# Optimization experiments

Measured on AMD Instinct MI355X. Metric: run time of the kernel, lower is better.

## Reference

```python
import jax, jax.numpy as jnp
import numpy as np

D = 12          # tree depth; N = 2**D - 1 = 4095 nodes per tree (heap layout)
B = 64          # batch of trees
V = 128         # VOCAB_SIZE (one-hot token width)
H = 256         # hidden_size
NUM_OPS = 20
TEMP = 3.0      # self.temperature


def setup_inputs() -> dict:
    key = jax.random.key(0)
    ks = jax.random.split(key, 9)
    s = 0.02
    return {
        "arg_hot": jax.random.uniform(ks[0], (B, 2**D - 1, V), dtype=jnp.float32),
        "Wiou": jax.random.normal(ks[1], (V, 3 * H), dtype=jnp.float32) * s,
        "biou": jnp.zeros((3 * H,), jnp.float32),
        "Uiou": jax.random.normal(ks[2], (2, H, 3 * H), dtype=jnp.float32) * s,
        "Wf": jax.random.normal(ks[3], (V, H), dtype=jnp.float32) * s,
        "bf": jnp.zeros((H,), jnp.float32),
        "Uf": jax.random.normal(ks[4], (2, 2, H, H), dtype=jnp.float32) * s,
        "actor_w": jax.random.normal(ks[5], (NUM_OPS, H), dtype=jnp.float32) * s,
        "actor_b": jnp.zeros((NUM_OPS,), jnp.float32),
        "validity_mask": jnp.ones((B, NUM_OPS), jnp.float32),
    }


def _binary_tree_lstm(arg_hot, Wiou, biou, Uiou, Wf, bf, Uf):
    """Levelized apply_binary_lstm: bottom-up N-ary (N=2) Tree-LSTM over a
    complete binary tree stored in heap order (children of node j at level l
    are positions 2j, 2j+1 of level l+1). Missing children (below leaves)
    contribute zero hidden/cell states, matching self.tz in the original."""
    Bn = arg_hot.shape[0]
    h_child = c_child = None
    h = c = None
    for l in reversed(range(D)):
        m = 2 ** l
        x = arg_hot[:, m - 1: 2 * m - 1]                    # [B, m, V]
        if h_child is None:  # leaf level: zero child states
            hk = jnp.zeros((2, Bn, m, H), arg_hot.dtype)
            ck = hk
        else:                # children 2j, 2j+1 are adjacent pairs
            hk = h_child.reshape(Bn, m, 2, H).transpose(2, 0, 1, 3)  # [2,B,m,H]
            ck = c_child.reshape(Bn, m, 2, H).transpose(2, 0, 1, 3)
        iou = (jnp.einsum('bmv,vg->bmg', x, Wiou) + biou
               + jnp.einsum('kbmh,khg->bmg', hk, Uiou))     # [B,m,3H]
        i, o, u = jnp.split(iou, 3, axis=-1)
        i, o, u = jax.nn.sigmoid(i), jax.nn.sigmoid(o), jnp.tanh(u)
        # per-child forget gates f_k = sigma(Wf x + sum_j Uf[k,j] h_j + bf)
        f = jax.nn.sigmoid(jnp.einsum('bmv,vh->bmh', x, Wf) + bf
                           + jnp.einsum('jbmh,kjhd->kbmd', hk, Uf))  # [2,B,m,H]
        c = i * u + jnp.sum(f * ck, axis=0)                 # [B,m,H]
        h = o * jnp.tanh(c)
        h_child, c_child = h, c
    return h[:, 0], c[:, 0]                                  # root states [B,H]


def reference(arg_hot, Wiou, biou, Uiou, Wf, bf, Uf, actor_w, actor_b, validity_mask):
    root_h, _ = _binary_tree_lstm(arg_hot, Wiou, biou, Uiou, Wf, bf, Uf)
    # external-actor branch of policy(): mask weights/bias, add log-mask, tempered softmax
    w = actor_w[None, :, :] * validity_mask[:, :, None]      # [B,O,H]
    b = actor_b[None, :] * validity_mask                     # [B,O]
    logits = jnp.log(validity_mask) + jnp.einsum('bh,boh->bo', root_h, w) + b
    return jax.nn.softmax(logits / TEMP, axis=-1)
```

## Files before the change

kernel.cpp:

```cpp
#include <hip/hip_runtime.h>
#include <hip/hip_bf16.h>
#include <math.h>

typedef __hip_bfloat16 bf16;
typedef float f32x4 __attribute__((ext_vector_type(4)));
typedef short bf16x8 __attribute__((ext_vector_type(8)));

#define NNODES 4095
#define BATCH 64
#define NUM_OPS 20
#define TEMP 3.0f

#define OFF_WTILE 0x000000ull
#define OFF_WTL   0x190000ull
#define OFF_BIAS  0x1C0000ull
#define OFF_HA    0x200000ull
#define OFF_CA    (OFF_HA + (64ull<<20))
#define OFF_HB    (OFF_CA + (64ull<<20))
#define OFF_CB    (OFF_HB + (32ull<<20))
#define OFF_XL    OFF_HB

__device__ __forceinline__ float sigmoid_f(float x) {
    return 1.0f / (1.0f + __expf(-x));
}
__device__ __forceinline__ float tanh_f(float x) {
    return 1.0f - 2.0f / (__expf(2.0f * x) + 1.0f);
}

__device__ __forceinline__ void async_copy16(const bf16* g, bf16* l) {
    __builtin_amdgcn_global_load_lds(
        (const __attribute__((address_space(1))) void*)g,
        (__attribute__((address_space(3))) void*)l,
        16, 0, 0);
}

__global__ void init_weights(const float* __restrict__ Wiou,
                             const float* __restrict__ biou,
                             const float* __restrict__ Uiou,
                             const float* __restrict__ Wf,
                             const float* __restrict__ bfv,
                             const float* __restrict__ Uf,
                             bf16* __restrict__ wtile,
                             bf16* __restrict__ wtL,
                             float* __restrict__ biasCat)
{
    int idx = blockIdx.x * 256 + threadIdx.x;
    if (idx < 1280 * 640) {
        int k = idx % 640;
        int n = idx / 640;
        int g = n >> 8;
        int ch = n & 255;
        float v;
        if (k < 128) {
            v = (g < 3) ? Wiou[k * 768 + n] : Wf[k * 256 + ch];
        } else {
            int par = (k < 384) ? 0 : 1;
            int hh = (k - 128) & 255;
            if (g < 3) v = Uiou[(par * 256 + hh) * 768 + n];
            else {
                int kk = g - 3;
                v = Uf[(((kk * 2 + par) * 256) + hh) * 256 + ch];
            }
        }
        bf16 bv = __float2bfloat16(v);
        int chblk = (ch >> 5);
        int cl    = ch & 31;
        int kb    = k >> 6;
        int chunk = (k & 63) >> 3;
        int e     = k & 7;
        int brow  = g * 32 + cl;
        wtile[((size_t)(chblk * 10 + kb) * 8 + chunk) * 1280 + brow * 8 + e] = bv;
        if (k < 128 && g < 3)
            wtL[((size_t)(chblk * 2 + kb) * 8 + chunk) * 768 + brow * 8 + e] = bv;
    }
    if (idx < 1280) {
        biasCat[idx] = (idx < 768) ? biou[idx] : bfv[idx & 255];
    }
}

__global__ void convert_x(const float* __restrict__ arg_hot, bf16* __restrict__ xL)
{
    int t = blockIdx.x * 256 + threadIdx.x;
    int row = t >> 4;
    int ch0 = (t & 15) * 8;
    int b = row >> 11;
    int j = row & 2047;
    const float* src = arg_hot + ((size_t)b * NNODES + 2047 + j) * 128 + ch0;
    float4 a = *(const float4*)src;
    float4 c = *(const float4*)(src + 4);
    union { bf16x8 v; __hip_bfloat162 h2[4]; } u;
    u.h2[0] = __float22bfloat162_rn(make_float2(a.x, a.y));
    u.h2[1] = __float22bfloat162_rn(make_float2(a.z, a.w));
    u.h2[2] = __float22bfloat162_rn(make_float2(c.x, c.y));
    u.h2[3] = __float22bfloat162_rn(make_float2(c.z, c.w));
    *(bf16x8*)(xL + (size_t)t * 8) = u.v;
}

template <bool LEAF>
__global__ __launch_bounds__(256, 2)
void level_kernel(const float* __restrict__ arg_hot,
                  const bf16* __restrict__ wt,
                  const float* __restrict__ biasCat,
                  const bf16* __restrict__ xL,
                  const bf16* __restrict__ h_child,
                  const bf16* __restrict__ c_child,
                  bf16* __restrict__ h_out,
                  bf16* __restrict__ c_out,
                  int m, int logm)
{
    constexpr int NG  = LEAF ? 3 : 5;
    constexpr int KI  = LEAF ? 2 : 10;
    constexpr int BR  = LEAF ? 96 : 160;
    constexpr int NBW = LEAF ? 3 : 5;

    const int M = BATCH * m;
    const int node_base = m - 1;

    __shared__ bf16 As[2][128 * 64];
    __shared__ bf16 Bs[2][8 * BR * 8];

    const int tid = threadIdx.x;

    int bid = blockIdx.x;
    int mtiles = gridDim.x >> 3;
    int mtile, chblk;
    if ((mtiles & 7) == 0) {
        int xcd = bid & 7;
        int seq = bid >> 3;
        chblk = seq & 7;
        mtile = ((seq >> 3) << 3) + xcd;
    } else {
        mtile = bid >> 3;
        chblk = bid & 7;
    }
    const int rbase  = mtile * 128;
    const int chbase = chblk * 32;

    const int lane = tid & 63;
    const int wave = tid >> 6;
    const int wr = wave & 1;
    const int wc = wave >> 1;
    const int l15 = lane & 15;
    const int lq  = lane >> 4;
    const int xr7 = l15 & 7;

    f32x4 acc[4][NG];
#pragma unroll
    for (int a = 0; a < 4; ++a)
#pragma unroll
        for (int g = 0; g < NG; ++g)
            acc[a][g] = (f32x4){0.f, 0.f, 0.f, 0.f};

    const int row_l = lane >> 3;
    const int cc_l  = lane & 7;
    const int aoffH = row_l * 512 + (cc_l ^ row_l) * 8;
    const int aoffX = row_l * 128 + (cc_l ^ row_l) * 8;

    const bf16* wbase = wt + (size_t)chblk * KI * (BR * 64);

    const int arow = tid & 127;
    const int rs = min(rbase + arow, M - 1);
    const float* xrow = LEAF ? nullptr : arg_hot +
        ((size_t)(rs >> logm) * NNODES + node_base + (rs & (m - 1))) * 128;
    const int xswz_base = arow * 64;
    const int ar7 = arow & 7;

    const bf16* xLbase = LEAF ? xL + (size_t)rbase * 128 + aoffX : nullptr;

    auto stage = [&](int kb, int buf) {
        bf16* Ab = As[buf];
        bf16* Bb = Bs[buf];
        if (LEAF) {
            const bf16* xb = xLbase + kb * 64;
#pragma unroll
            for (int i = 0; i < 4; ++i) {
                int t = wave * 4 + i;
                async_copy16(xb + t * 1024, &Ab[t * 512]);
            }
        } else if (kb < 2) {
            const float* xk = xrow + kb * 64;
#pragma unroll
            for (int j = 0; j < 4; ++j) {
                int chunk = (tid >> 7) + 2 * j;
                const float* src = xk + chunk * 8;
                float4 a = *(const float4*)src;
                float4 b = *(const float4*)(src + 4);
                union { int4 i4; __hip_bfloat162 h2[4]; } u;
                u.h2[0] = __float22bfloat162_rn(make_float2(a.x, a.y));
                u.h2[1] = __float22bfloat162_rn(make_float2(a.z, a.w));
                u.h2[2] = __float22bfloat162_rn(make_float2(b.x, b.y));
                u.h2[3] = __float22bfloat162_rn(make_float2(b.z, b.w));
                *(int4*)&Ab[xswz_base + ((chunk ^ ar7) * 8)] = u.i4;
            }
        } else {
            const bf16* hb = h_child + (size_t)rbase * 512 + (kb * 64 - 128) + aoffH;
#pragma unroll
            for (int i = 0; i < 4; ++i) {
                int t = wave * 4 + i;
                async_copy16(hb + t * 8 * 512, &Ab[t * 512]);
            }
        }
        const bf16* bsrc = wbase + (size_t)kb * (BR * 64);
#pragma unroll
        for (int i = 0; i < NBW; ++i) {
            int t = wave * NBW + i;
            async_copy16(bsrc + t * 512 + lane * 8, &Bb[t * 512]);
        }
    };

    stage(0, 0);

    for (int kb = 0; kb < KI; ++kb) {
        int buf = kb & 1;
        __syncthreads();
        if (kb + 1 < KI) stage(kb + 1, buf ^ 1);
#pragma unroll
        for (int ks = 0; ks < 2; ++ks) {
            int q = ks * 4 + lq;
            int qa = (q ^ xr7) * 8;
            bf16x8 af[4];
#pragma unroll
            for (int rt = 0; rt < 4; ++rt)
                af[rt] = *(const bf16x8*)&As[buf][(wr * 64 + rt * 16 + l15) * 64 + qa];
#pragma unroll
            for (int g = 0; g < NG; ++g) {
                bf16x8 bfr = *(const bf16x8*)&Bs[buf][q * (BR * 8) + (g * 32 + wc * 16 + l15) * 8];
#pragma unroll
                for (int rt = 0; rt < 4; ++rt)
                    acc[rt][g] = __builtin_amdgcn_mfma_f32_16x16x32_bf16(
                        af[rt], bfr, acc[rt][g], 0, 0, 0);
            }
        }
    }

    const int ch = chbase + wc * 16 + l15;
    const float b_i = biasCat[ch];
    const float b_o = biasCat[256 + ch];
    const float b_u = biasCat[512 + ch];
    const float b_f = LEAF ? 0.f : biasCat[768 + ch];

#pragma unroll
    for (int rt = 0; rt < 4; ++rt) {
#pragma unroll
        for (int ri = 0; ri < 4; ++ri) {
            int r = rbase + wr * 64 + rt * 16 + lq * 4 + ri;
            if (r < M) {
                float i = sigmoid_f(acc[rt][0][ri] + b_i);
                float o = sigmoid_f(acc[rt][1][ri] + b_o);
                float u = tanh_f(acc[rt][2][ri] + b_u);
                float cn;
                if (LEAF) {
                    cn = i * u;
                } else {
                    float f0 = sigmoid_f(acc[rt][3][ri] + b_f);
                    float f1 = sigmoid_f(acc[rt][4][ri] + b_f);
                    float c0 = __bfloat162float(c_child[(size_t)r * 512 + ch]);
                    float c1 = __bfloat162float(c_child[(size_t)r * 512 + 256 + ch]);
                    cn = i * u + f0 * c0 + f1 * c1;
                }
                float h = o * tanh_f(cn);
                h_out[(size_t)r * 256 + ch] = __float2bfloat16(h);
                c_out[(size_t)r * 256 + ch] = __float2bfloat16(cn);
            }
        }
    }
}

__global__ void head_kernel(const bf16* __restrict__ rootH,
                            const float* __restrict__ actor_w,
                            const float* __restrict__ actor_b,
                            const float* __restrict__ vmask,
                            float* __restrict__ out)
{
    int b = blockIdx.x;
    __shared__ float logits[NUM_OPS];
    int t = threadIdx.x;
    if (t < NUM_OPS) {
        const bf16* hr = rootH + b * 256;
        const float* w = actor_w + t * 256;
        float dot = 0.f;
        for (int hh = 0; hh < 256; ++hh)
            dot += __bfloat162float(hr[hh]) * w[hh];
        float mk = vmask[b * NUM_OPS + t];
        float lg = (mk > 0.f) ? (logf(mk) + (dot + actor_b[t]) * mk) : -INFINITY;
        logits[t] = lg / TEMP;
    }
    __syncthreads();
    if (t == 0) {
        float mx = -INFINITY;
        for (int o = 0; o < NUM_OPS; ++o) mx = fmaxf(mx, logits[o]);
        float s = 0.f;
        float e[NUM_OPS];
        for (int o = 0; o < NUM_OPS; ++o) { e[o] = __expf(logits[o] - mx); s += e[o]; }
        float inv = 1.f / s;
        for (int o = 0; o < NUM_OPS; ++o) out[b * NUM_OPS + o] = e[o] * inv;
    }
}

extern "C" void kernel_launch(void* const* d_in, const int* in_sizes, int n_in,
                              void* d_out, int out_size, void* d_ws, size_t ws_size,
                              hipStream_t stream)
{
    const float* arg_hot = (const float*)d_in[0];
    const float* Wiou    = (const float*)d_in[1];
    const float* biou    = (const float*)d_in[2];
    const float* Uiou    = (const float*)d_in[3];
    const float* Wf      = (const float*)d_in[4];
    const float* bfv     = (const float*)d_in[5];
    const float* Uf      = (const float*)d_in[6];
    const float* actor_w = (const float*)d_in[7];
    const float* actor_b = (const float*)d_in[8];
    const float* vmask   = (const float*)d_in[9];

    char* ws = (char*)d_ws;
    bf16*  wtile   = (bf16*)(ws + OFF_WTILE);
    bf16*  wtL     = (bf16*)(ws + OFF_WTL);
    float* biasCat = (float*)(ws + OFF_BIAS);
    bf16*  hA = (bf16*)(ws + OFF_HA);
    bf16*  cA = (bf16*)(ws + OFF_CA);
    bf16*  hB = (bf16*)(ws + OFF_HB);
    bf16*  cB = (bf16*)(ws + OFF_CB);
    bf16*  xL = (bf16*)(ws + OFF_XL);

    init_weights<<<dim3((1280 * 640 + 255) / 256), 256, 0, stream>>>(
        Wiou, biou, Uiou, Wf, bfv, Uf, wtile, wtL, biasCat);
    convert_x<<<dim3(8192), 256, 0, stream>>>(arg_hot, xL);

    {
        int m = 2048;
        int mtiles = (BATCH * m + 127) / 128;
        level_kernel<true><<<dim3(mtiles * 8), 256, 0, stream>>>(
            arg_hot, wtL, biasCat, xL, nullptr, nullptr, hA, cA, m, 11);
    }
    for (int l = 10; l >= 0; --l) {
        int m = 1 << l;
        int mtiles = (BATCH * m + 127) / 128;
        bf16 *hc, *cc, *ho, *co;
        if (l & 1) { hc = hB; cc = cB; ho = hA; co = cA; }
        else       { hc = hA; cc = cA; ho = hB; co = cB; }
        level_kernel<false><<<dim3(mtiles * 8), 256, 0, stream>>>(
            arg_hot, wtile, biasCat, nullptr, hc, cc, ho, co, m, l);
    }
    head_kernel<<<dim3(BATCH), 64, 0, stream>>>(hB, actor_w, actor_b, vmask, (float*)d_out);
}
```

Before: 835.1 us.

## Split gate groups across two wave groups in 512-thread level kernel

Doubles the level kernel block to 512 threads. One group of four waves computes the i/o/u gate GEMMs and the other computes the two forget gates (for leaves: i,u vs o). Partial results are exchanged through shared memory reused from the A tile, with an extra barrier in the epilogue. The aim is to cut the accumulator registers per wave and raise the number of resident waves for latency hiding. The cost is an uneven 3:2 split of MFMA work, an extra barrier, and shared-memory traffic in the epilogue.

```diff
diff --git a/kernel.cpp b/kernel.cpp
--- a/kernel.cpp
+++ b/kernel.cpp
@@ -97,7 +97,7 @@
 }
 
 template <bool LEAF>
-__global__ __launch_bounds__(256, 2)
+__global__ __launch_bounds__(512, 4)
 void level_kernel(const float* __restrict__ arg_hot,
                   const bf16* __restrict__ wt,
                   const float* __restrict__ biasCat,
@@ -108,10 +108,11 @@
                   bf16* __restrict__ c_out,
                   int m, int logm)
 {
-    constexpr int NG  = LEAF ? 3 : 5;
     constexpr int KI  = LEAF ? 2 : 10;
     constexpr int BR  = LEAF ? 96 : 160;
-    constexpr int NBW = LEAF ? 3 : 5;
+    constexpr int BI  = LEAF ? 12 : 20;
+    constexpr int NG0 = LEAF ? 2 : 3;
+    constexpr int NG1 = LEAF ? 1 : 2;
 
     const int M = BATCH * m;
     const int node_base = m - 1;
@@ -139,16 +140,17 @@
     const int lane = tid & 63;
     const int wave = tid >> 6;
     const int wr = wave & 1;
-    const int wc = wave >> 1;
+    const int wc = (wave >> 1) & 1;
+    const int wg = wave >> 2;
     const int l15 = lane & 15;
     const int lq  = lane >> 4;
     const int xr7 = l15 & 7;
 
-    f32x4 acc[4][NG];
+    f32x4 acc[4][3];
 #pragma unroll
     for (int a = 0; a < 4; ++a)
 #pragma unroll
-        for (int g = 0; g < NG; ++g)
+        for (int g = 0; g < 3; ++g)
             acc[a][g] = (f32x4){0.f, 0.f, 0.f, 0.f};
 
     const int row_l = lane >> 3;
@@ -173,15 +175,15 @@
         if (LEAF) {
             const bf16* xb = xLbase + kb * 64;
 #pragma unroll
-            for (int i = 0; i < 4; ++i) {
-                int t = wave * 4 + i;
+            for (int jj = 0; jj < 2; ++jj) {
+                int t = wave * 2 + jj;
                 async_copy16(xb + t * 1024, &Ab[t * 512]);
             }
         } else if (kb < 2) {
             const float* xk = xrow + kb * 64;
 #pragma unroll
-            for (int j = 0; j < 4; ++j) {
-                int chunk = (tid >> 7) + 2 * j;
+            for (int jj = 0; jj < 2; ++jj) {
+                int chunk = (tid >> 7) + 4 * jj;
                 const float* src = xk + chunk * 8;
                 float4 a = *(const float4*)src;
                 float4 b = *(const float4*)(src + 4);
@@ -195,17 +197,14 @@
         } else {
             const bf16* hb = h_child + (size_t)rbase * 512 + (kb * 64 - 128) + aoffH;
 #pragma unroll
-            for (int i = 0; i < 4; ++i) {
-                int t = wave * 4 + i;
+            for (int jj = 0; jj < 2; ++jj) {
+                int t = wave * 2 + jj;
                 async_copy16(hb + t * 8 * 512, &Ab[t * 512]);
             }
         }
         const bf16* bsrc = wbase + (size_t)kb * (BR * 64);
-#pragma unroll
-        for (int i = 0; i < NBW; ++i) {
-            int t = wave * NBW + i;
-            async_copy16(bsrc + t * 512 + lane * 8, &Bb[t * 512]);
-        }
+        for (int j = wave; j < BI; j += 8)
+            async_copy16(bsrc + j * 512 + lane * 8, &Bb[j * 512]);
     };
 
     stage(0, 0);
@@ -222,46 +221,108 @@
 #pragma unroll
             for (int rt = 0; rt < 4; ++rt)
                 af[rt] = *(const bf16x8*)&As[buf][(wr * 64 + rt * 16 + l15) * 64 + qa];
-#pragma unroll
-            for (int g = 0; g < NG; ++g) {
-                bf16x8 bfr = *(const bf16x8*)&Bs[buf][q * (BR * 8) + (g * 32 + wc * 16 + l15) * 8];
-#pragma unroll
-                for (int rt = 0; rt < 4; ++rt)
-                    acc[rt][g] = __builtin_amdgcn_mfma_f32_16x16x32_bf16(
-                        af[rt], bfr, acc[rt][g], 0, 0, 0);
+            if (wg == 0) {
+#pragma unroll
+                for (int gi = 0; gi < NG0; ++gi) {
+                    int g = LEAF ? gi * 2 : gi;
+                    bf16x8 bfr = *(const bf16x8*)&Bs[buf][q * (BR * 8) + (g * 32 + wc * 16 + l15) * 8];
+#pragma unroll
+                    for (int rt = 0; rt < 4; ++rt)
+                        acc[rt][gi] = __builtin_amdgcn_mfma_f32_16x16x32_bf16(
+                            af[rt], bfr, acc[rt][gi], 0, 0, 0);
+                }
+            } else {
+#pragma unroll
+                for (int gi = 0; gi < NG1; ++gi) {
+                    int g = LEAF ? 1 : 3 + gi;
+                    bf16x8 bfr = *(const bf16x8*)&Bs[buf][q * (BR * 8) + (g * 32 + wc * 16 + l15) * 8];
+#pragma unroll
+                    for (int rt = 0; rt < 4; ++rt)
+                        acc[rt][gi] = __builtin_amdgcn_mfma_f32_16x16x32_bf16(
+                            af[rt], bfr, acc[rt][gi], 0, 0, 0);
+                }
             }
         }
     }
 
     const int ch = chbase + wc * 16 + l15;
-    const float b_i = biasCat[ch];
-    const float b_o = biasCat[256 + ch];
-    const float b_u = biasCat[512 + ch];
-    const float b_f = LEAF ? 0.f : biasCat[768 + ch];
-
-#pragma unroll
-    for (int rt = 0; rt < 4; ++rt) {
-#pragma unroll
-        for (int ri = 0; ri < 4; ++ri) {
-            int r = rbase + wr * 64 + rt * 16 + lq * 4 + ri;
-            if (r < M) {
-                float i = sigmoid_f(acc[rt][0][ri] + b_i);
-                float o = sigmoid_f(acc[rt][1][ri] + b_o);
-                float u = tanh_f(acc[rt][2][ri] + b_u);
-                float cn;
-                if (LEAF) {
-                    cn = i * u;
-                } else {
-                    float f0 = sigmoid_f(acc[rt][3][ri] + b_f);
-                    float f1 = sigmoid_f(acc[rt][4][ri] + b_f);
-                    float c0 = __bfloat162float(c_child[(size_t)r * 512 + ch]);
-                    float c1 = __bfloat162float(c_child[(size_t)r * 512 + 256 + ch]);
-                    cn = i * u + f0 * c0 + f1 * c1;
-                }
-                float h = o * tanh_f(cn);
-                h_out[(size_t)r * 256 + ch] = __float2bfloat16(h);
-                c_out[(size_t)r * 256 + ch] = __float2bfloat16(cn);
-            }
+    float* fs = (float*)(&As[0][0]);
+    const int sbase = (wr * 2 + wc) * 64 + lane;
+
+    if (!LEAF) {
+        if (wg == 1) {
+            const float b_f = biasCat[768 + ch];
+#pragma unroll
+            for (int rt = 0; rt < 4; ++rt)
+#pragma unroll
+                for (int ri = 0; ri < 4; ++ri) {
+                    int r = rbase + wr * 64 + rt * 16 + lq * 4 + ri;
+                    float v = 0.f;
+                    if (r < M) {
+                        float f0 = sigmoid_f(acc[rt][0][ri] + b_f);
+                        float f1 = sigmoid_f(acc[rt][1][ri] + b_f);
+                        float c0 = __bfloat162float(c_child[(size_t)r * 512 + ch]);
+                        float c1 = __bfloat162float(c_child[(size_t)r * 512 + 256 + ch]);
+                        v = f0 * c0 + f1 * c1;
+                    }
+                    fs[(rt * 4 + ri) * 256 + sbase] = v;
+                }
+        }
+        __syncthreads();
+        if (wg == 0) {
+            const float b_i = biasCat[ch];
+            const float b_o = biasCat[256 + ch];
+            const float b_u = biasCat[512 + ch];
+#pragma unroll
+            for (int rt = 0; rt < 4; ++rt)
+#pragma unroll
+                for (int ri = 0; ri < 4; ++ri) {
+                    int r = rbase + wr * 64 + rt * 16 + lq * 4 + ri;
+                    if (r < M) {
+                        float i = sigmoid_f(acc[rt][0][ri] + b_i);
+                        float o = sigmoid_f(acc[rt][1][ri] + b_o);
+                        float u = tanh_f(acc[rt][2][ri] + b_u);
+                        float cn = i * u + fs[(rt * 4 + ri) * 256 + sbase];
+                        float h = o * tanh_f(cn);
+                        h_out[(size_t)r * 256 + ch] = __float2bfloat16(h);
+                        c_out[(size_t)r * 256 + ch] = __float2bfloat16(cn);
+                    }
+                }
+        }
+    } else {
+        if (wg == 0) {
+            const float b_i = biasCat[ch];
+            const float b_u = biasCat[512 + ch];
+#pragma unroll
+            for (int rt = 0; rt < 4; ++rt)
+#pragma unroll
+                for (int ri = 0; ri < 4; ++ri) {
+                    int r = rbase + wr * 64 + rt * 16 + lq * 4 + ri;
+                    float cn = 0.f;
+                    if (r < M) {
+                        float i = sigmoid_f(acc[rt][0][ri] + b_i);
+                        float u = tanh_f(acc[rt][1][ri] + b_u);
+                        cn = i * u;
+                        c_out[(size_t)r * 256 + ch] = __float2bfloat16(cn);
+                    }
+                    fs[(rt * 4 + ri) * 256 + sbase] = cn;
+                }
+        }
+        __syncthreads();
+        if (wg == 1) {
+            const float b_o = biasCat[256 + ch];
+#pragma unroll
+            for (int rt = 0; rt < 4; ++rt)
+#pragma unroll
+                for (int ri = 0; ri < 4; ++ri) {
+                    int r = rbase + wr * 64 + rt * 16 + lq * 4 + ri;
+                    if (r < M) {
+                        float o = sigmoid_f(acc[rt][0][ri] + b_o);
+                        float cn = fs[(rt * 4 + ri) * 256 + sbase];
+                        float h = o * tanh_f(cn);
+                        h_out[(size_t)r * 256 + ch] = __float2bfloat16(h);
+                    }
+                }
         }
     }
 }
@@ -329,7 +390,7 @@
     {
         int m = 2048;
         int mtiles = (BATCH * m + 127) / 128;
-        level_kernel<true><<<dim3(mtiles * 8), 256, 0, stream>>>(
+        level_kernel<true><<<dim3(mtiles * 8), 512, 0, stream>>>(
             arg_hot, wtL, biasCat, xL, nullptr, nullptr, hA, cA, m, 11);
     }
     for (int l = 10; l >= 0; --l) {
@@ -338,7 +399,7 @@
         bf16 *hc, *cc, *ho, *co;
         if (l & 1) { hc = hB; cc = cB; ho = hA; co = cA; }
         else       { hc = hA; cc = cA; ho = hB; co = cB; }
-        level_kernel<false><<<dim3(mtiles * 8), 256, 0, stream>>>(
+        level_kernel<false><<<dim3(mtiles * 8), 512, 0, stream>>>(
             arg_hot, wtile, biasCat, nullptr, hc, cc, ho, co, m, l);
     }
     head_kernel<<<dim3(BATCH), 64, 0, stream>>>(hB, actor_w, actor_b, vmask, (float*)d_out);
```

Result: slower. 984.3 us (+17.9%).

## Halve K tile to 32 and shrink LDS to allow four blocks per CU

Applied to the files above, without the earlier changes.

Halves the K-dimension tile from 64 to 32. The weight tiles are repacked into matching 32-wide chunks, the A-tile swizzle is reworked for 32-element rows, and shared-memory buffers are halved. Launch bounds are raised from 2 to 4 blocks per CU so more waves can hide memory latency. The cost is twice as many pipeline iterations and barriers per GEMM, and a tighter register budget that could cause spills given the 20-accumulator array.

```diff
diff --git a/kernel.cpp b/kernel.cpp
--- a/kernel.cpp
+++ b/kernel.cpp
@@ -65,13 +65,13 @@
         bf16 bv = __float2bfloat16(v);
         int chblk = (ch >> 5);
         int cl    = ch & 31;
-        int kb    = k >> 6;
-        int chunk = (k & 63) >> 3;
+        int kb    = k >> 5;
+        int chunk = (k & 31) >> 3;
         int e     = k & 7;
         int brow  = g * 32 + cl;
-        wtile[((size_t)(chblk * 10 + kb) * 8 + chunk) * 1280 + brow * 8 + e] = bv;
+        wtile[((size_t)(chblk * 20 + kb) * 4 + chunk) * 1280 + brow * 8 + e] = bv;
         if (k < 128 && g < 3)
-            wtL[((size_t)(chblk * 2 + kb) * 8 + chunk) * 768 + brow * 8 + e] = bv;
+            wtL[((size_t)(chblk * 4 + kb) * 4 + chunk) * 768 + brow * 8 + e] = bv;
     }
     if (idx < 1280) {
         biasCat[idx] = (idx < 768) ? biou[idx] : bfv[idx & 255];
@@ -97,7 +97,7 @@
 }
 
 template <bool LEAF>
-__global__ __launch_bounds__(256, 2)
+__global__ __launch_bounds__(256, 4)
 void level_kernel(const float* __restrict__ arg_hot,
                   const bf16* __restrict__ wt,
                   const float* __restrict__ biasCat,
@@ -109,15 +109,15 @@
                   int m, int logm)
 {
     constexpr int NG  = LEAF ? 3 : 5;
-    constexpr int KI  = LEAF ? 2 : 10;
+    constexpr int KI  = LEAF ? 4 : 20;
     constexpr int BR  = LEAF ? 96 : 160;
-    constexpr int NBW = LEAF ? 3 : 5;
+    constexpr int BI  = LEAF ? 6 : 10;
 
     const int M = BATCH * m;
     const int node_base = m - 1;
 
-    __shared__ bf16 As[2][128 * 64];
-    __shared__ bf16 Bs[2][8 * BR * 8];
+    __shared__ bf16 As[2][128 * 32];
+    __shared__ bf16 Bs[2][4 * BR * 8];
 
     const int tid = threadIdx.x;
 
@@ -142,7 +142,7 @@
     const int wc = wave >> 1;
     const int l15 = lane & 15;
     const int lq  = lane >> 4;
-    const int xr7 = l15 & 7;
+    const int xr3 = (l15 >> 1) & 3;
 
     f32x4 acc[4][NG];
 #pragma unroll
@@ -151,19 +151,19 @@
         for (int g = 0; g < NG; ++g)
             acc[a][g] = (f32x4){0.f, 0.f, 0.f, 0.f};
 
-    const int row_l = lane >> 3;
-    const int cc_l  = lane & 7;
-    const int aoffH = row_l * 512 + (cc_l ^ row_l) * 8;
-    const int aoffX = row_l * 128 + (cc_l ^ row_l) * 8;
-
-    const bf16* wbase = wt + (size_t)chblk * KI * (BR * 64);
+    const int l4 = lane >> 2;
+    const int c4 = lane & 3;
+    const int akey  = (l4 >> 1) & 3;
+    const int aoffH = l4 * 512 + (c4 ^ akey) * 8;
+    const int aoffX = l4 * 128 + (c4 ^ akey) * 8;
+
+    const bf16* wbase = wt + (size_t)chblk * KI * (BR * 32);
 
     const int arow = tid & 127;
     const int rs = min(rbase + arow, M - 1);
     const float* xrow = LEAF ? nullptr : arg_hot +
         ((size_t)(rs >> logm) * NNODES + node_base + (rs & (m - 1))) * 128;
-    const int xswz_base = arow * 64;
-    const int ar7 = arow & 7;
+    const int ar3 = (arow >> 1) & 3;
 
     const bf16* xLbase = LEAF ? xL + (size_t)rbase * 128 + aoffX : nullptr;
 
@@ -171,18 +171,18 @@
         bf16* Ab = As[buf];
         bf16* Bb = Bs[buf];
         if (LEAF) {
-            const bf16* xb = xLbase + kb * 64;
-#pragma unroll
-            for (int i = 0; i < 4; ++i) {
-                int t = wave * 4 + i;
-                async_copy16(xb + t * 1024, &Ab[t * 512]);
-            }
-        } else if (kb < 2) {
-            const float* xk = xrow + kb * 64;
-#pragma unroll
-            for (int j = 0; j < 4; ++j) {
-                int chunk = (tid >> 7) + 2 * j;
-                const float* src = xk + chunk * 8;
+            const bf16* xb = xLbase + kb * 32;
+#pragma unroll
+            for (int i = 0; i < 2; ++i) {
+                int t = wave * 2 + i;
+                async_copy16(xb + t * 2048, &Ab[t * 512]);
+            }
+        } else if (kb < 4) {
+            const float* xk = xrow + kb * 32;
+#pragma unroll
+            for (int j = 0; j < 2; ++j) {
+                int c = (tid >> 7) + 2 * j;
+                const float* src = xk + c * 8;
                 float4 a = *(const float4*)src;
                 float4 b = *(const float4*)(src + 4);
                 union { int4 i4; __hip_bfloat162 h2[4]; } u;
@@ -190,22 +190,19 @@
                 u.h2[1] = __float22bfloat162_rn(make_float2(a.z, a.w));
                 u.h2[2] = __float22bfloat162_rn(make_float2(b.x, b.y));
                 u.h2[3] = __float22bfloat162_rn(make_float2(b.z, b.w));
-                *(int4*)&Ab[xswz_base + ((chunk ^ ar7) * 8)] = u.i4;
+                *(int4*)&Ab[arow * 32 + ((c ^ ar3) * 8)] = u.i4;
             }
         } else {
-            const bf16* hb = h_child + (size_t)rbase * 512 + (kb * 64 - 128) + aoffH;
-#pragma unroll
-            for (int i = 0; i < 4; ++i) {
-                int t = wave * 4 + i;
-                async_copy16(hb + t * 8 * 512, &Ab[t * 512]);
+            const bf16* hb = h_child + (size_t)rbase * 512 + (kb * 32 - 128) + aoffH;
+#pragma unroll
+            for (int i = 0; i < 2; ++i) {
+                int t = wave * 2 + i;
+                async_copy16(hb + (size_t)t * 16 * 512, &Ab[t * 512]);
             }
         }
-        const bf16* bsrc = wbase + (size_t)kb * (BR * 64);
-#pragma unroll
-        for (int i = 0; i < NBW; ++i) {
-            int t = wave * NBW + i;
-            async_copy16(bsrc + t * 512 + lane * 8, &Bb[t * 512]);
-        }
+        const bf16* bsrc = wbase + (size_t)kb * (BR * 32);
+        for (int j = wave; j < BI; j += 4)
+            async_copy16(bsrc + j * 512 + lane * 8, &Bb[j * 512]);
     };
 
     stage(0, 0);
@@ -214,22 +211,17 @@
         int buf = kb & 1;
         __syncthreads();
         if (kb + 1 < KI) stage(kb + 1, buf ^ 1);
-#pragma unroll
-        for (int ks = 0; ks < 2; ++ks) {
-            int q = ks * 4 + lq;
-            int qa = (q ^ xr7) * 8;
-            bf16x8 af[4];
+        bf16x8 af[4];
+#pragma unroll
+        for (int rt = 0; rt < 4; ++rt)
+            af[rt] = *(const bf16x8*)&As[buf][(wr * 64 + rt * 16 + l15) * 32 + ((lq ^ xr3) * 8)];
+#pragma unroll
+        for (int g = 0; g < NG; ++g) {
+            bf16x8 bfr = *(const bf16x8*)&Bs[buf][lq * (BR * 8) + (g * 32 + wc * 16 + l15) * 8];
 #pragma unroll
             for (int rt = 0; rt < 4; ++rt)
-                af[rt] = *(const bf16x8*)&As[buf][(wr * 64 + rt * 16 + l15) * 64 + qa];
-#pragma unroll
-            for (int g = 0; g < NG; ++g) {
-                bf16x8 bfr = *(const bf16x8*)&Bs[buf][q * (BR * 8) + (g * 32 + wc * 16 + l15) * 8];
-#pragma unroll
-                for (int rt = 0; rt < 4; ++rt)
-                    acc[rt][g] = __builtin_amdgcn_mfma_f32_16x16x32_bf16(
-                        af[rt], bfr, acc[rt][g], 0, 0, 0);
-            }
+                acc[rt][g] = __builtin_amdgcn_mfma_f32_16x16x32_bf16(
+                    af[rt], bfr, acc[rt][g], 0, 0, 0);
         }
     }
 
```

Result: faster. 802.4 us (-3.9%).

## Load weight fragments directly from global into registers, drop B shared-memory staging

Applied to the files above, without the earlier changes.

Reorders the pre-tiled weight buffer so each lane's MFMA B-fragment is a contiguous 16-byte chunk. Each wave then loads its fragments straight from global memory (L2-cached) into registers instead of async-copying them into LDS. This removes the B tile's LDS footprint and LDS traffic and raises the occupancy hint to 3 blocks per SM. In exchange, every wave issues global loads inside the k-loop that are not prefetched a stage ahead, which may expose latency. The extra fragment registers may also fight the higher occupancy target.

```diff
diff --git a/kernel.cpp b/kernel.cpp
--- a/kernel.cpp
+++ b/kernel.cpp
@@ -63,15 +63,17 @@
             }
         }
         bf16 bv = __float2bfloat16(v);
-        int chblk = (ch >> 5);
-        int cl    = ch & 31;
+        int chblk = ch >> 5;
+        int wc    = (ch >> 4) & 1;
+        int l15   = ch & 15;
         int kb    = k >> 6;
-        int chunk = (k & 63) >> 3;
+        int ks    = (k >> 5) & 1;
+        int lq    = (k >> 3) & 3;
         int e     = k & 7;
-        int brow  = g * 32 + cl;
-        wtile[((size_t)(chblk * 10 + kb) * 8 + chunk) * 1280 + brow * 8 + e] = bv;
+        int inner = l15 * 32 + lq * 8 + e;
+        wtile[(size_t)(((((chblk * 10 + kb) * 2 + ks) * 5 + g) * 2 + wc)) * 512 + inner] = bv;
         if (k < 128 && g < 3)
-            wtL[((size_t)(chblk * 2 + kb) * 8 + chunk) * 768 + brow * 8 + e] = bv;
+            wtL[(size_t)(((((chblk * 2 + kb) * 2 + ks) * 3 + g) * 2 + wc)) * 512 + inner] = bv;
     }
     if (idx < 1280) {
         biasCat[idx] = (idx < 768) ? biou[idx] : bfv[idx & 255];
@@ -97,7 +99,7 @@
 }
 
 template <bool LEAF>
-__global__ __launch_bounds__(256, 2)
+__global__ __launch_bounds__(256, 3)
 void level_kernel(const float* __restrict__ arg_hot,
                   const bf16* __restrict__ wt,
                   const float* __restrict__ biasCat,
@@ -110,14 +112,11 @@
 {
     constexpr int NG  = LEAF ? 3 : 5;
     constexpr int KI  = LEAF ? 2 : 10;
-    constexpr int BR  = LEAF ? 96 : 160;
-    constexpr int NBW = LEAF ? 3 : 5;
 
     const int M = BATCH * m;
     const int node_base = m - 1;
 
     __shared__ bf16 As[2][128 * 64];
-    __shared__ bf16 Bs[2][8 * BR * 8];
 
     const int tid = threadIdx.x;
 
@@ -156,7 +155,8 @@
     const int aoffH = row_l * 512 + (cc_l ^ row_l) * 8;
     const int aoffX = row_l * 128 + (cc_l ^ row_l) * 8;
 
-    const bf16* wbase = wt + (size_t)chblk * KI * (BR * 64);
+    const bf16* bptr = wt + ((size_t)chblk * KI * 2 * NG * 2 + wc) * 512
+                          + l15 * 32 + lq * 8;
 
     const int arow = tid & 127;
     const int rs = min(rbase + arow, M - 1);
@@ -167,9 +167,8 @@
 
     const bf16* xLbase = LEAF ? xL + (size_t)rbase * 128 + aoffX : nullptr;
 
-    auto stage = [&](int kb, int buf) {
+    auto stageA = [&](int kb, int buf) {
         bf16* Ab = As[buf];
-        bf16* Bb = Bs[buf];
         if (LEAF) {
             const bf16* xb = xLbase + kb * 64;
 #pragma unroll
@@ -200,36 +199,34 @@
                 async_copy16(hb + t * 8 * 512, &Ab[t * 512]);
             }
         }
-        const bf16* bsrc = wbase + (size_t)kb * (BR * 64);
-#pragma unroll
-        for (int i = 0; i < NBW; ++i) {
-            int t = wave * NBW + i;
-            async_copy16(bsrc + t * 512 + lane * 8, &Bb[t * 512]);
-        }
     };
 
-    stage(0, 0);
+    stageA(0, 0);
 
     for (int kb = 0; kb < KI; ++kb) {
         int buf = kb & 1;
         __syncthreads();
-        if (kb + 1 < KI) stage(kb + 1, buf ^ 1);
+        if (kb + 1 < KI) stageA(kb + 1, buf ^ 1);
+        bf16x8 fbr[2][NG];
+#pragma unroll
+        for (int ks = 0; ks < 2; ++ks)
+#pragma unroll
+            for (int g = 0; g < NG; ++g)
+                fbr[ks][g] = *(const bf16x8*)(bptr +
+                    (size_t)(((kb * 2 + ks) * NG + g) * 2) * 512);
 #pragma unroll
         for (int ks = 0; ks < 2; ++ks) {
-            int q = ks * 4 + lq;
-            int qa = (q ^ xr7) * 8;
+            int qa = ((ks * 4 + lq) ^ xr7) * 8;
             bf16x8 af[4];
 #pragma unroll
             for (int rt = 0; rt < 4; ++rt)
                 af[rt] = *(const bf16x8*)&As[buf][(wr * 64 + rt * 16 + l15) * 64 + qa];
 #pragma unroll
-            for (int g = 0; g < NG; ++g) {
-                bf16x8 bfr = *(const bf16x8*)&Bs[buf][q * (BR * 8) + (g * 32 + wc * 16 + l15) * 8];
+            for (int g = 0; g < NG; ++g)
 #pragma unroll
                 for (int rt = 0; rt < 4; ++rt)
                     acc[rt][g] = __builtin_amdgcn_mfma_f32_16x16x32_bf16(
-                        af[rt], bfr, acc[rt][g], 0, 0, 0);
-            }
+                        af[rt], fbr[ks][g], acc[rt][g], 0, 0, 0);
         }
     }
 
```

After: 849.9 us. Within noise of the previous version (+1.8%).
